# Performance work log

Hardware: AMD Instinct MI355X
Metric: run time of the kernel (lower is better)

## Reference

```python
import jax, jax.numpy as jnp
import numpy as np

NUM_FEAS = 4096
HID = 128
BATCH = 128


def setup_inputs() -> dict:
    key = jax.random.key(0)
    k1, k2, k3, k4 = jax.random.split(key, 4)
    batch_x = jax.random.normal(k1, (BATCH, NUM_FEAS), dtype=jnp.float32)
    C = jax.random.normal(k2, (1, HID), dtype=jnp.float32)
    W = jax.random.normal(k3, (NUM_FEAS, HID), dtype=jnp.float32)
    B = jax.random.normal(k4, (NUM_FEAS,), dtype=jnp.float32)
    return {"batch_x": batch_x, "C": C, "W": W, "B": B}


def reference(batch_x, C, W, B):
    # binarize input (matches (x > 0).float())
    x = (batch_x > 0).astype(jnp.float32)  # [B, F]
    # prefix sums: S_excl[b, i] = sum_{j < i} x[b, j] * W[j]   -> [B, F, H]
    contrib = x[:, :, None] * W[None, :, :]
    S = jnp.cumsum(contrib, axis=1)
    S_excl = jnp.concatenate([jnp.zeros_like(S[:, :1]), S[:, :-1]], axis=1)
    # hidden state for i >= 1: h_i = sigmoid(S_excl_i + C)
    h = jax.nn.sigmoid(S_excl + C[None, :, :])  # [B, F, H]
    # faithful quirk: for i == 0 the original uses raw C (no sigmoid)
    h = h.at[:, 0, :].set(jnp.broadcast_to(C[0], (x.shape[0], HID)))
    # logits z_i = h_i . W_i + B_i ; p_i = sigmoid(z_i)
    z = jnp.einsum('bfh,fh->bf', h, W) + B[None, :]
    # BCE(sum over features), stable via log_sigmoid
    log_p = jax.nn.log_sigmoid(z)
    log_q = jax.nn.log_sigmoid(-z)
    loss_per_sample = -jnp.sum(x * log_p + (1.0 - x) * log_q, axis=1)
    return jnp.mean(loss_per_sample)
```

## Files before the change

kernel.cpp:

```cpp
#include <hip/hip_runtime.h>

#define NFEAS 4096
#define HID   128
#define BATCH 128
#define NSUB  64
#define NC    16
#define KF    256
#define L2E   1.4426950408889634f
#define LN2   0.6931471805599453f

__device__ __forceinline__ float scan64(float v) {
  float r = v; int y;
  y = __builtin_amdgcn_update_dpp(0, __float_as_int(r), 0x111, 0xF, 0xF, true); r += __int_as_float(y);
  y = __builtin_amdgcn_update_dpp(0, __float_as_int(r), 0x112, 0xF, 0xF, true); r += __int_as_float(y);
  y = __builtin_amdgcn_update_dpp(0, __float_as_int(r), 0x114, 0xF, 0xF, true); r += __int_as_float(y);
  y = __builtin_amdgcn_update_dpp(0, __float_as_int(r), 0x118, 0xF, 0xF, true); r += __int_as_float(y);
  y = __builtin_amdgcn_update_dpp(0, __float_as_int(r), 0x142, 0xA, 0xF, true); r += __int_as_float(y);
  y = __builtin_amdgcn_update_dpp(0, __float_as_int(r), 0x143, 0xC, 0xF, true); r += __int_as_float(y);
  return r;
}

__global__ __launch_bounds__(64) void chunk_sums_kernel(
    const float* __restrict__ x, const float* __restrict__ W,
    float* __restrict__ T)
{
  const int b = blockIdx.x, c = blockIdx.y, t = threadIdx.x;
  const int base = c * 64;
  const unsigned long long m = __ballot(x[(size_t)b * NFEAS + base + t] > 0.f);
  float s0 = 0.f, s1 = 0.f;
  for (int i = 0; i < 64; ++i) {
    if ((m >> (unsigned)i) & 1ull) {
      const float* wr = W + (size_t)(base + i) * HID;
      s0 += wr[t];
      s1 += wr[64 + t];
    }
  }
  T[((size_t)b * HID + t) * NSUB + c]      = s0;
  T[((size_t)b * HID + t + 64) * NSUB + c] = s1;
}

__global__ __launch_bounds__(256) void prefix_kernel(float* __restrict__ T)
{
  const int gw = blockIdx.x * 4 + (threadIdx.x >> 6);
  const int lane = threadIdx.x & 63;
  float* p = T + (size_t)gw * NSUB;
  const float v = p[lane];
  const float r = scan64(v);
  p[lane] = r - v;
}

__global__ __launch_bounds__(512, 6) void scan_loss_kernel(
    const float* __restrict__ x,  const float* __restrict__ Cv,
    const float* __restrict__ W,  const float* __restrict__ Bv,
    const float* __restrict__ T,  float* __restrict__ losses)
{
  __shared__ float wt[32 * 256];
  __shared__ float s2m[HID];
  __shared__ float s2r[HID];
  __shared__ float lred[8];

  const int tid = threadIdx.x;
  const int b = blockIdx.x, c = blockIdx.y;
  const int base = c * KF;
  const int lane = tid & 63, w = tid >> 6;

  if (tid < HID) {
    const float s2 = T[((size_t)b * HID + tid) * NSUB + c * 4] + Cv[tid];
    s2r[tid] = s2;
    s2m[tid] = -L2E * s2;
  }

  const float4 xv = *reinterpret_cast<const float4*>(
      x + (size_t)b * NFEAS + base + 4 * lane);
  const float xm0 = xv.x > 0.f ? 1.f : 0.f;
  const float xm1 = xv.y > 0.f ? 1.f : 0.f;
  const float xm2 = xv.z > 0.f ? 1.f : 0.f;
  const float xm3 = xv.w > 0.f ? 1.f : 0.f;

  float z0 = 0.f, z1 = 0.f, z2 = 0.f, z3 = 0.f;

  const int fst = tid & 255;
  const int hh2 = tid >> 8;
  const float* wrow = W + (size_t)(base + fst) * HID;
  const bool quirk = (c == 0);

  for (int hq = 0; hq < 4; ++hq) {
    if (hq) __syncthreads();
    #pragma unroll
    for (int k = 0; k < 4; ++k) {
      const float4 v = *reinterpret_cast<const float4*>(
          wrow + hq * 32 + hh2 * 16 + k * 4);
      const int h = hh2 * 16 + k * 4;
      wt[(h + 0) * 256 + fst] = v.x;
      wt[(h + 1) * 256 + fst] = v.y;
      wt[(h + 2) * 256 + fst] = v.z;
      wt[(h + 3) * 256 + fst] = v.w;
    }
    __syncthreads();
    #pragma unroll
    for (int j = 0; j < 4; ++j) {
      const int hl = w * 4 + j;
      const int h  = hq * 32 + hl;
      const float4 wv = *reinterpret_cast<const float4*>(&wt[hl * 256 + 4 * lane]);
      const float mw0 = wv.x * xm0, mw1 = wv.y * xm1;
      const float mw2 = wv.z * xm2, mw3 = wv.w * xm3;
      const float ps = (mw0 + mw1) + (mw2 + mw3);
      const float r  = scan64(ps);
      const float e0 = r - ps;
      const float e1 = e0 + mw0;
      const float e2 = e1 + mw1;
      const float e3 = e2 + mw2;
      const float sm = s2m[h];
      float g0 = __builtin_amdgcn_rcpf(1.f + __builtin_amdgcn_exp2f(__builtin_fmaf(e0, -L2E, sm)));
      float g1 = __builtin_amdgcn_rcpf(1.f + __builtin_amdgcn_exp2f(__builtin_fmaf(e1, -L2E, sm)));
      float g2 = __builtin_amdgcn_rcpf(1.f + __builtin_amdgcn_exp2f(__builtin_fmaf(e2, -L2E, sm)));
      float g3 = __builtin_amdgcn_rcpf(1.f + __builtin_amdgcn_exp2f(__builtin_fmaf(e3, -L2E, sm)));
      if (quirk && lane == 0) g0 = s2r[h];
      z0 = __builtin_fmaf(g0, wv.x, z0);
      z1 = __builtin_fmaf(g1, wv.y, z1);
      z2 = __builtin_fmaf(g2, wv.z, z2);
      z3 = __builtin_fmaf(g3, wv.w, z3);
    }
  }

  __syncthreads();
  {
    float4 zv; zv.x = z0; zv.y = z1; zv.z = z2; zv.w = z3;
    *reinterpret_cast<float4*>(&wt[w * 256 + 4 * lane]) = zv;
  }
  __syncthreads();

  if (tid < 256) {
    float zt = 0.f;
    #pragma unroll
    for (int ww = 0; ww < 8; ++ww) zt += wt[ww * 256 + tid];
    zt += Bv[base + tid];
    const float xf = x[(size_t)b * NFEAS + base + tid] > 0.f ? 1.f : 0.f;
    const float az = __builtin_fabsf(zt);
    const float ee = __builtin_amdgcn_exp2f(-L2E * az);
    const float li = fmaxf(zt, 0.f) - xf * zt +
                     LN2 * __builtin_amdgcn_logf(1.f + ee);
    const float tot = scan64(li);
    if ((tid & 63) == 63) lred[tid >> 6] = tot;
  }
  __syncthreads();
  if (tid == 0)
    losses[b * NC + c] = (lred[0] + lred[1]) + (lred[2] + lred[3]);
}

__global__ __launch_bounds__(256) void finalize_kernel(
    const float* __restrict__ losses, float* __restrict__ out)
{
  __shared__ float sm[256];
  const int t = threadIdx.x;
  float s = 0.f;
  for (int i = t; i < BATCH * NC; i += 256) s += losses[i];
  sm[t] = s;
  __syncthreads();
  for (int w = 128; w > 0; w >>= 1) {
    if (t < w) sm[t] += sm[t + w];
    __syncthreads();
  }
  if (t == 0) out[0] = sm[0] * (1.f / BATCH);
}

extern "C" void kernel_launch(void* const* d_in, const int* in_sizes, int n_in,
                              void* d_out, int out_size, void* d_ws, size_t ws_size,
                              hipStream_t stream)
{
  const float* x  = (const float*)d_in[0];
  const float* Cv = (const float*)d_in[1];
  const float* W  = (const float*)d_in[2];
  const float* Bv = (const float*)d_in[3];
  float* out = (float*)d_out;

  float* T      = (float*)d_ws;
  float* losses = T + (size_t)BATCH * HID * NSUB;

  chunk_sums_kernel<<<dim3(BATCH, NSUB), 64, 0, stream>>>(x, W, T);
  prefix_kernel<<<dim3(BATCH * HID / 4), 256, 0, stream>>>(T);
  scan_loss_kernel<<<dim3(BATCH, NC), 512, 0, stream>>>(x, Cv, W, Bv, T, losses);
  finalize_kernel<<<1, 256, 0, stream>>>(losses, out);
}
```

Measured before the change: 64.96 us.

## Batch chunk sums over 8 samples, swizzle LDS transpose, interleave four DPP scans

```diff
diff --git a/kernel.cpp b/kernel.cpp
--- a/kernel.cpp
+++ b/kernel.cpp
@@ -20,23 +20,59 @@
   return r;
 }
 
-__global__ __launch_bounds__(64) void chunk_sums_kernel(
+__device__ __forceinline__ void scan64_x4(float& a, float& b, float& c, float& d) {
+  int t0, t1, t2, t3;
+#define S4(ctrl, rm)                                                              \
+  t0 = __builtin_amdgcn_update_dpp(0, __float_as_int(a), ctrl, rm, 0xF, true);    \
+  t1 = __builtin_amdgcn_update_dpp(0, __float_as_int(b), ctrl, rm, 0xF, true);    \
+  t2 = __builtin_amdgcn_update_dpp(0, __float_as_int(c), ctrl, rm, 0xF, true);    \
+  t3 = __builtin_amdgcn_update_dpp(0, __float_as_int(d), ctrl, rm, 0xF, true);    \
+  a += __int_as_float(t0); b += __int_as_float(t1);                               \
+  c += __int_as_float(t2); d += __int_as_float(t3);
+  S4(0x111, 0xF) S4(0x112, 0xF) S4(0x114, 0xF) S4(0x118, 0xF)
+  S4(0x142, 0xA) S4(0x143, 0xC)
+#undef S4
+}
+
+__global__ __launch_bounds__(128) void chunk_sums_kernel(
     const float* __restrict__ x, const float* __restrict__ W,
     float* __restrict__ T)
 {
-  const int b = blockIdx.x, c = blockIdx.y, t = threadIdx.x;
-  const int base = c * 64;
-  const unsigned long long m = __ballot(x[(size_t)b * NFEAS + base + t] > 0.f);
-  float s0 = 0.f, s1 = 0.f;
-  for (int i = 0; i < 64; ++i) {
-    if ((m >> (unsigned)i) & 1ull) {
-      const float* wr = W + (size_t)(base + i) * HID;
-      s0 += wr[t];
-      s1 += wr[64 + t];
-    }
-  }
-  T[((size_t)b * HID + t) * NSUB + c]      = s0;
-  T[((size_t)b * HID + t + 64) * NSUB + c] = s1;
+  __shared__ float xm[64][8];
+  const int c = blockIdx.x, g = blockIdx.y, t = threadIdx.x;
+
+  {
+    const int s = t >> 4, fb = (t & 15) << 2;
+    const float4 v = *reinterpret_cast<const float4*>(
+        &x[(size_t)(g * 8 + s) * NFEAS + c * 64 + fb]);
+    xm[fb + 0][s] = v.x > 0.f ? 1.f : 0.f;
+    xm[fb + 1][s] = v.y > 0.f ? 1.f : 0.f;
+    xm[fb + 2][s] = v.z > 0.f ? 1.f : 0.f;
+    xm[fb + 3][s] = v.w > 0.f ? 1.f : 0.f;
+  }
+  __syncthreads();
+
+  float acc[8];
+  #pragma unroll
+  for (int s = 0; s < 8; ++s) acc[s] = 0.f;
+
+  #pragma unroll 4
+  for (int f = 0; f < 64; ++f) {
+    const float wv = W[(size_t)(c * 64 + f) * HID + t];
+    const float4 ma = *reinterpret_cast<const float4*>(&xm[f][0]);
+    const float4 mb = *reinterpret_cast<const float4*>(&xm[f][4]);
+    acc[0] = __builtin_fmaf(ma.x, wv, acc[0]);
+    acc[1] = __builtin_fmaf(ma.y, wv, acc[1]);
+    acc[2] = __builtin_fmaf(ma.z, wv, acc[2]);
+    acc[3] = __builtin_fmaf(ma.w, wv, acc[3]);
+    acc[4] = __builtin_fmaf(mb.x, wv, acc[4]);
+    acc[5] = __builtin_fmaf(mb.y, wv, acc[5]);
+    acc[6] = __builtin_fmaf(mb.z, wv, acc[6]);
+    acc[7] = __builtin_fmaf(mb.w, wv, acc[7]);
+  }
+  #pragma unroll
+  for (int s = 0; s < 8; ++s)
+    T[((size_t)(g * 8 + s) * HID + t) * NSUB + c] = acc[s];
 }
 
 __global__ __launch_bounds__(256) void prefix_kernel(float* __restrict__ T)
@@ -49,7 +85,7 @@
   p[lane] = r - v;
 }
 
-__global__ __launch_bounds__(512, 6) void scan_loss_kernel(
+__global__ __launch_bounds__(512, 4) void scan_loss_kernel(
     const float* __restrict__ x,  const float* __restrict__ Cv,
     const float* __restrict__ W,  const float* __restrict__ Bv,
     const float* __restrict__ T,  float* __restrict__ losses)
@@ -79,48 +115,69 @@
 
   float z0 = 0.f, z1 = 0.f, z2 = 0.f, z3 = 0.f;
 
-  const int fst = tid & 255;
-  const int hh2 = tid >> 8;
-  const float* wrow = W + (size_t)(base + fst) * HID;
+  const int hb = tid & 7;
+  const int f0 = tid >> 3;
+  const int colw = f0 ^ ((hb & 3) << 3);
+  const float* wbase = W + (size_t)base * HID;
   const bool quirk = (c == 0);
 
   for (int hq = 0; hq < 4; ++hq) {
     if (hq) __syncthreads();
     #pragma unroll
     for (int k = 0; k < 4; ++k) {
+      const int f = f0 + (k << 6);
       const float4 v = *reinterpret_cast<const float4*>(
-          wrow + hq * 32 + hh2 * 16 + k * 4);
-      const int h = hh2 * 16 + k * 4;
-      wt[(h + 0) * 256 + fst] = v.x;
-      wt[(h + 1) * 256 + fst] = v.y;
-      wt[(h + 2) * 256 + fst] = v.z;
-      wt[(h + 3) * 256 + fst] = v.w;
+          wbase + (size_t)f * HID + (hq << 5) + (hb << 2));
+      float* wp = &wt[((hb << 2) << 8) + colw + (k << 6)];
+      wp[0]   = v.x;
+      wp[256] = v.y;
+      wp[512] = v.z;
+      wp[768] = v.w;
     }
     __syncthreads();
-    #pragma unroll
-    for (int j = 0; j < 4; ++j) {
-      const int hl = w * 4 + j;
-      const int h  = hq * 32 + hl;
-      const float4 wv = *reinterpret_cast<const float4*>(&wt[hl * 256 + 4 * lane]);
-      const float mw0 = wv.x * xm0, mw1 = wv.y * xm1;
-      const float mw2 = wv.z * xm2, mw3 = wv.w * xm3;
-      const float ps = (mw0 + mw1) + (mw2 + mw3);
-      const float r  = scan64(ps);
-      const float e0 = r - ps;
-      const float e1 = e0 + mw0;
-      const float e2 = e1 + mw1;
-      const float e3 = e2 + mw2;
-      const float sm = s2m[h];
-      float g0 = __builtin_amdgcn_rcpf(1.f + __builtin_amdgcn_exp2f(__builtin_fmaf(e0, -L2E, sm)));
-      float g1 = __builtin_amdgcn_rcpf(1.f + __builtin_amdgcn_exp2f(__builtin_fmaf(e1, -L2E, sm)));
-      float g2 = __builtin_amdgcn_rcpf(1.f + __builtin_amdgcn_exp2f(__builtin_fmaf(e2, -L2E, sm)));
-      float g3 = __builtin_amdgcn_rcpf(1.f + __builtin_amdgcn_exp2f(__builtin_fmaf(e3, -L2E, sm)));
-      if (quirk && lane == 0) g0 = s2r[h];
-      z0 = __builtin_fmaf(g0, wv.x, z0);
-      z1 = __builtin_fmaf(g1, wv.y, z1);
-      z2 = __builtin_fmaf(g2, wv.z, z2);
-      z3 = __builtin_fmaf(g3, wv.w, z3);
+
+    const int hl0 = w << 2;
+    const int colx = (lane << 2) ^ ((w & 3) << 3);
+    const float4 wv0 = *reinterpret_cast<const float4*>(&wt[(hl0 + 0) * 256 + colx]);
+    const float4 wv1 = *reinterpret_cast<const float4*>(&wt[(hl0 + 1) * 256 + colx]);
+    const float4 wv2 = *reinterpret_cast<const float4*>(&wt[(hl0 + 2) * 256 + colx]);
+    const float4 wv3 = *reinterpret_cast<const float4*>(&wt[(hl0 + 3) * 256 + colx]);
+    const float4 sm4 = *reinterpret_cast<const float4*>(&s2m[(hq << 5) + hl0]);
+
+    const float m00 = wv0.x * xm0, m01 = wv0.y * xm1, m02 = wv0.z * xm2, m03 = wv0.w * xm3;
+    const float m10 = wv1.x * xm0, m11 = wv1.y * xm1, m12 = wv1.z * xm2, m13 = wv1.w * xm3;
+    const float m20 = wv2.x * xm0, m21 = wv2.y * xm1, m22 = wv2.z * xm2, m23 = wv2.w * xm3;
+    const float m30 = wv3.x * xm0, m31 = wv3.y * xm1, m32 = wv3.z * xm2, m33 = wv3.w * xm3;
+
+    const float ps0 = (m00 + m01) + (m02 + m03);
+    const float ps1 = (m10 + m11) + (m12 + m13);
+    const float ps2 = (m20 + m21) + (m22 + m23);
+    const float ps3 = (m30 + m31) + (m32 + m33);
+
+    float r0 = ps0, r1 = ps1, r2 = ps2, r3 = ps3;
+    scan64_x4(r0, r1, r2, r3);
+
+#define CHAIN(J, wvJ, rJ, psJ, mJ0, mJ1, mJ2, smJ)                                          \
+    {                                                                                        \
+      const float e0 = rJ - psJ;                                                             \
+      const float e1 = e0 + mJ0;                                                             \
+      const float e2 = e1 + mJ1;                                                             \
+      const float e3 = e2 + mJ2;                                                             \
+      float g0 = __builtin_amdgcn_rcpf(1.f + __builtin_amdgcn_exp2f(__builtin_fmaf(e0, -L2E, smJ))); \
+      const float g1 = __builtin_amdgcn_rcpf(1.f + __builtin_amdgcn_exp2f(__builtin_fmaf(e1, -L2E, smJ))); \
+      const float g2 = __builtin_amdgcn_rcpf(1.f + __builtin_amdgcn_exp2f(__builtin_fmaf(e2, -L2E, smJ))); \
+      const float g3 = __builtin_amdgcn_rcpf(1.f + __builtin_amdgcn_exp2f(__builtin_fmaf(e3, -L2E, smJ))); \
+      if (quirk && lane == 0) g0 = s2r[(hq << 5) + hl0 + J];                                 \
+      z0 = __builtin_fmaf(g0, wvJ.x, z0);                                                    \
+      z1 = __builtin_fmaf(g1, wvJ.y, z1);                                                    \
+      z2 = __builtin_fmaf(g2, wvJ.z, z2);                                                    \
+      z3 = __builtin_fmaf(g3, wvJ.w, z3);                                                    \
     }
+    CHAIN(0, wv0, r0, ps0, m00, m01, m02, sm4.x)
+    CHAIN(1, wv1, r1, ps1, m10, m11, m12, sm4.y)
+    CHAIN(2, wv2, r2, ps2, m20, m21, m22, sm4.z)
+    CHAIN(3, wv3, r3, ps3, m30, m31, m32, sm4.w)
+#undef CHAIN
   }
 
   __syncthreads();
@@ -177,7 +234,7 @@
   float* T      = (float*)d_ws;
   float* losses = T + (size_t)BATCH * HID * NSUB;
 
-  chunk_sums_kernel<<<dim3(BATCH, NSUB), 64, 0, stream>>>(x, W, T);
+  chunk_sums_kernel<<<dim3(NSUB, BATCH / 8), 128, 0, stream>>>(x, W, T);
   prefix_kernel<<<dim3(BATCH * HID / 4), 256, 0, stream>>>(T);
   scan_loss_kernel<<<dim3(BATCH, NC), 512, 0, stream>>>(x, Cv, W, Bv, T, losses);
   finalize_kernel<<<1, 256, 0, stream>>>(losses, out);
```

After: 55.24 us. 15.0% less time.
